# Kernel optimization log

Hardware: AMD Instinct MI355X
Metric: run time of the kernel (lower is better)

The kernel has to match this reference:

```python
import jax, jax.numpy as jnp
import numpy as np

B, S, D_EMBED, D_HIDDEN = 4, 256, 300, 300
C = 5.0  # frozen tanh-scaling constant


def setup_inputs() -> dict:
    key = jax.random.key(0)
    ks = jax.random.split(key, 8)
    w = 0.05  # ~xavier scale for 300x300
    return {
        "inputs": jax.random.normal(ks[0], (B, S, D_EMBED), jnp.float32),
        "rep_mask": jax.random.randint(ks[1], (B, S), 0, 2, jnp.int32),
        "W_fc": jax.random.normal(ks[2], (D_HIDDEN, D_EMBED), jnp.float32) * w,
        "b_fc": jnp.zeros((D_HIDDEN,), jnp.float32),
        "W1": jax.random.normal(ks[3], (D_HIDDEN, D_HIDDEN), jnp.float32) * w,
        "W2": jax.random.normal(ks[4], (D_HIDDEN, D_HIDDEN), jnp.float32) * w,
        "b1": jnp.zeros((D_HIDDEN,), jnp.float32),
        "W_f1": jax.random.normal(ks[5], (D_HIDDEN, D_HIDDEN), jnp.float32) * w,
        "W_f2": jax.random.normal(ks[6], (D_HIDDEN, D_HIDDEN), jnp.float32) * w,
        "b_f": jnp.zeros((D_HIDDEN,), jnp.float32),
    }


def _disa_fwd(inputs, rep_mask_f, W_fc, b_fc, W1, W2, b1, W_f1, W_f2, b_f):
    n_seq = inputs.shape[1]
    # forward direction mask: attend to strictly later positions (triu, diag=1)
    direct = jnp.triu(jnp.ones((n_seq, n_seq), inputs.dtype), k=1)
    # mask[b,i,j] = rep_mask[b,j] * direct[i,j], shape [B,S,S,1]
    mask = (rep_mask_f[:, None, :] * direct[None]) [..., None]

    rep_map = jax.nn.elu(jnp.einsum('bse,he->bsh', inputs, W_fc) + b_fc)  # [B,S,D]
    dep = jnp.einsum('bsh,gh->bsg', rep_map, W1)   # dependent (token j)
    head = jnp.einsum('bsh,gh->bsg', rep_map, W2)  # head (token i)

    # logits[b,i,j,d]
    logits = C * jnp.tanh((dep[:, None, :, :] + head[:, :, None, :] + b1) / C)

    # hand-rolled masked softmax over dim=2 (j), faithful to original
    masked = logits * mask
    mx = jnp.max(masked, axis=2, keepdims=True)
    exps = jnp.exp(masked - mx) * mask
    sums = jnp.sum(exps, axis=2, keepdims=True)
    sums = sums + (sums == 0).astype(logits.dtype)
    attn = (exps / (sums + 1e-20)) * mask

    attn_result = jnp.sum(attn * rep_map[:, None, :, :], axis=2)  # [B,S,D]

    gate = jax.nn.sigmoid(
        jnp.einsum('bsh,gh->bsg', rep_map, W_f1)
        + jnp.einsum('bsh,gh->bsg', attn_result, W_f2)
        + b_f
    )
    out = gate * rep_map + (1.0 - gate) * attn_result
    return out * rep_mask_f[..., None]


def reference(inputs, rep_mask, W_fc, b_fc, W1, W2, b1, W_f1, W_f2, b_f):
    rep_mask_f = rep_mask.astype(inputs.dtype)
    return _disa_fwd(inputs, rep_mask_f, W_fc, b_fc, W1, W2, b1, W_f1, W_f2, b_f)
```

## Files before the change

kernel.cpp:

```cpp
#include <hip/hip_runtime.h>
#include <hip/hip_bf16.h>

#define Dx 300

#define REPF   0
#define ED     307200
#define HEADF  921600
#define U_BASE 1228800
#define REPB   0
#define ATB    327680
#define WPACK  655360
#define WP1    655360
#define WP2    757760
#define WPF1   860160
#define WPF2   962560
#define ATTNF  1761280
#define SYNC_FOFF 2100000

typedef __attribute__((ext_vector_type(8))) short short8;
typedef __attribute__((ext_vector_type(4))) float f32x4;

union S8 { unsigned int u[4]; unsigned short s[8]; short8 v; };

__device__ __forceinline__ float bf2f(unsigned short u) {
    union { unsigned int i; float f; } v; v.i = ((unsigned int)u) << 16; return v.f;
}
__device__ __forceinline__ unsigned short f2bf(float x) {
    union { float f; unsigned int i; } u; u.f = x;
    return (unsigned short)((u.i + 0x8000u) >> 16);
}
__device__ __forceinline__ int detect_bf16(const void* w) {
    const unsigned short* u = (const unsigned short*)w;
    int ok = 1;
    #pragma unroll
    for (int t = 0; t < 64; ++t) { float v = bf2f(u[t]); ok &= (fabsf(v) < 1.0f) ? 1 : 0; }
    return ok;
}
__device__ __forceinline__ float ldf(const void* p, int idx, int isbf) {
    return isbf ? bf2f(((const unsigned short*)p)[idx]) : ((const float*)p)[idx];
}

__device__ __forceinline__ void st_wt_f32(float* p, float v) {
    asm volatile("global_store_dword %0, %1, off sc0 sc1"
                 :: "v"(p), "v"(v) : "memory");
}
__device__ __forceinline__ void st_wt_u16(unsigned short* p, unsigned short v) {
    unsigned int vv = v;
    asm volatile("global_store_short %0, %1, off sc0 sc1"
                 :: "v"(p), "v"(vv) : "memory");
}
__device__ __forceinline__ void st_wt_u32(void* p, unsigned int v) {
    asm volatile("global_store_dword %0, %1, off sc0 sc1"
                 :: "v"(p), "v"(v) : "memory");
}

__device__ __forceinline__ void load8f(const float* rowp, int kb, int kmax,
                                       int valid, float* x) {
    if (valid && kb + 8 <= kmax) {
        float4 a = *(const float4*)(rowp + kb);
        float4 b = *(const float4*)(rowp + kb + 4);
        x[0]=a.x; x[1]=a.y; x[2]=a.z; x[3]=a.w;
        x[4]=b.x; x[5]=b.y; x[6]=b.z; x[7]=b.w;
    } else {
        #pragma unroll
        for (int j = 0; j < 8; ++j) {
            int k = kb + j;
            x[j] = (valid && k < kmax) ? rowp[k] : 0.f;
        }
    }
}
__device__ __forceinline__ short8 pack8(const float* x) {
    S8 H;
    #pragma unroll
    for (int p = 0; p < 4; ++p) {
        union { float f; unsigned int i; } a, b;
        a.f = x[2*p]; b.f = x[2*p+1];
        H.u[p] = ((a.i + 0x8000u) >> 16) | ((b.i + 0x8000u) & 0xFFFF0000u);
    }
    return H.v;
}
__device__ __forceinline__ short8 load8bf(const unsigned short* rowp, int kb,
                                          int kmax, int valid) {
    S8 R;
    if (valid && kb + 8 <= kmax) {
        ushort4 a = *(const ushort4*)(rowp + kb);
        ushort4 b = *(const ushort4*)(rowp + kb + 4);
        R.s[0]=a.x; R.s[1]=a.y; R.s[2]=a.z; R.s[3]=a.w;
        R.s[4]=b.x; R.s[5]=b.y; R.s[6]=b.z; R.s[7]=b.w;
    } else {
        #pragma unroll
        for (int j = 0; j < 8; ++j) {
            int k = kb + j;
            R.s[j] = (valid && k < kmax) ? rowp[k] : (unsigned short)0;
        }
    }
    return R.v;
}
__device__ __forceinline__ short8 loadB(const void* W, int row, int kb, int isbf,
                                        int valid) {
    if (isbf) return load8bf((const unsigned short*)W + row * 300, kb, 300, valid);
    float t[8];
    load8f((const float*)W + row * 300, kb, 300, valid, t);
    return pack8(t);
}

#define AG __HIP_MEMORY_SCOPE_AGENT
__device__ __forceinline__ int xcd_id() {
    int x;
    asm volatile("s_getreg_b32 %0, hwreg(HW_REG_XCC_ID)" : "=s"(x));
    return x & 7;
}
__device__ __forceinline__ void gbar(float* ws, int idx, int nblk) {
    __syncthreads();
    if (threadIdx.x == 0) {
        int* base  = (int*)(ws + SYNC_FOFF) + idx * 2048;
        int* xcnt  = base;
        int* xflag = base + 8 * 64;
        const int xid = xcd_id();
        int t2 = __hip_atomic_fetch_add(xcnt + xid * 64, 1, __ATOMIC_RELAXED, AG);
        if (t2 == 0) {
            int t = 0;
            for (;;) {
                int s = 0;
                #pragma unroll
                for (int k = 0; k < 8; ++k)
                    s += __hip_atomic_load(xcnt + k * 64, __ATOMIC_RELAXED, AG);
                if (s >= nblk) break;
                __builtin_amdgcn_s_sleep(1);
                if (++t > 400000) break;
            }
            __hip_atomic_store(xflag + xid * 64, 1, __ATOMIC_RELAXED, AG);
        } else {
            int t = 0;
            while (__hip_atomic_load(xflag + xid * 64, __ATOMIC_RELAXED, AG) == 0) {
                __builtin_amdgcn_s_sleep(2);
                if (++t > 400000) break;
            }
        }
        asm volatile("" ::: "memory");
    }
    __syncthreads();
}

__global__ __launch_bounds__(320, 4) void k_a(
        const void* __restrict__ Xv, const void* __restrict__ Wfc,
        const void* __restrict__ bfc, const void* __restrict__ W1,
        const void* __restrict__ W2,  const void* __restrict__ b1v,
        const void* __restrict__ Wf1, const void* __restrict__ Wf2,
        float* __restrict__ ws) {
    __shared__ int s_isbf;
    const int tid = threadIdx.x;
    const int blk = blockIdx.x;
    if (tid == 0) s_isbf = detect_bf16(Wfc);
    __syncthreads();
    const int isbf = s_isbf;
    unsigned short* U = (unsigned short*)(ws + U_BASE);

    {
        const int g0 = blk * 640 + tid * 2;
        const int mi = g0 / 102400;
        const int rem = g0 - mi * 102400;
        const int row = rem / 320, k0 = rem - row * 320;
        const void* src = (mi == 0) ? W1 : (mi == 1) ? W2 : (mi == 2) ? Wf1 : Wf2;
        float v0 = (row < 300 && k0     < 300) ? ldf(src, row * 300 + k0,     isbf) : 0.f;
        float v1 = (row < 300 && k0 + 1 < 300) ? ldf(src, row * 300 + k0 + 1, isbf) : 0.f;
        unsigned int pk = (unsigned int)f2bf(v0) | ((unsigned int)f2bf(v1) << 16);
        st_wt_u32(U + WPACK + g0, pk);
    }
    if (blk < 320 && tid < 256) {
        const int w = tid >> 6, l = tid & 63;
        const int mt = blk / 5, nt = blk % 5;
        const int m0 = mt * 16, lm = l & 15, koff = (l >> 4) * 8;
        const int nrow = nt * 64 + w * 16 + lm;
        const int bval = nrow < 300;
        const int ncl = bval ? nrow : 0;
        f32x4 acc = {0.f, 0.f, 0.f, 0.f};
        if (isbf) {
            const unsigned short* Xp = (const unsigned short*)Xv + (m0 + lm) * 300;
            #pragma unroll
            for (int ks = 0; ks < 10; ++ks) {
                short8 a = load8bf(Xp, ks*32 + koff, 300, 1);
                short8 b = loadB(Wfc, ncl, ks*32 + koff, 1, bval);
                acc = __builtin_amdgcn_mfma_f32_16x16x32_bf16(a, b, acc, 0, 0, 0);
            }
        } else {
            const float* Xp = (const float*)Xv + (m0 + lm) * 300;
            #pragma unroll
            for (int ks = 0; ks < 10; ++ks) {
                float t[8]; load8f(Xp, ks*32 + koff, 300, 1, t);
                short8 a = pack8(t);
                short8 b = loadB(Wfc, ncl, ks*32 + koff, 0, bval);
                acc = __builtin_amdgcn_mfma_f32_16x16x32_bf16(a, b, acc, 0, 0, 0);
            }
        }
        if (bval) {
            float bb = ldf(bfc, nrow, isbf);
            #pragma unroll
            for (int r = 0; r < 4; ++r) {
                int mg = m0 + (l >> 4) * 4 + r;
                float v = acc[r] + bb;
                v = v > 0.f ? v : (__expf(v) - 1.f);
                ws[REPF + mg * 300 + nrow] = v;
                ws[ED + (mg * 300 + nrow) * 2 + 1] = v;
                st_wt_u16(U + REPB + mg * 320 + nrow, f2bf(v));
            }
        } else {
            #pragma unroll
            for (int r = 0; r < 4; ++r) {
                int mg = m0 + (l >> 4) * 4 + r;
                st_wt_u16(U + REPB + mg * 320 + nrow, 0);
            }
        }
    }
    gbar(ws, 0, 640);

    if (tid < 256) {
        const int w = tid >> 6, l = tid & 63;
        const int lm = l & 15, koff = (l >> 4) * 8;
        const int u = blk;
        const int mt = u / 10, nt = u % 10;
        const int m0 = mt * 16;
        const int ng = nt * 64 + w * 16 + lm;
        const int wsel = ng < 320;
        const int wrow = wsel ? ng : ng - 320;
        const unsigned short* ap = U + REPB + (m0 + lm) * 320 + koff;
        const unsigned short* bp = U + (wsel ? WP1 : WP2) + wrow * 320 + koff;
        f32x4 acc = {0.f, 0.f, 0.f, 0.f};
        #pragma unroll
        for (int ks = 0; ks < 10; ++ks) {
            short8 a = *(const short8*)(ap + ks * 32);
            short8 b = *(const short8*)(bp + ks * 32);
            acc = __builtin_amdgcn_mfma_f32_16x16x32_bf16(a, b, acc, 0, 0, 0);
        }
        if (ng < 300) {
            float bb = ldf(b1v, ng, isbf);
            #pragma unroll
            for (int r = 0; r < 4; ++r) {
                int mg = m0 + (l >> 4) * 4 + r;
                ws[ED + (mg * 300 + ng) * 2] = __expf(0.4f * (acc[r] + bb));
            }
        } else if (ng >= 320 && ng < 620) {
            #pragma unroll
            for (int r = 0; r < 4; ++r) {
                int mg = m0 + (l >> 4) * 4 + r;
                ws[HEADF + mg * 300 + (ng - 320)] = acc[r];
            }
        }
    }
}

__global__ __launch_bounds__(320, 4) void k_b(
        const int* __restrict__ mask, const void* __restrict__ Wfc,
        const void* __restrict__ bfv, float* __restrict__ ws,
        void* __restrict__ outv) {
    __shared__ int s_isbf;
    __shared__ unsigned short vlist[256];
    __shared__ int s_cnt, s_st0, s_st1;
    const int tid = threadIdx.x;
    const int blk = blockIdx.x;
    if (tid == 0) s_isbf = detect_bf16(Wfc);
    __syncthreads();
    const int isbf = s_isbf;
    unsigned short* U = (unsigned short*)(ws + U_BASE);

    {
        const int b = blk >> 7;
        const int tile = blk & 127;
        const int uu = tile >> 1;
        const int i0 = (tile & 1) ? (254 - 2 * uu) : (2 * uu);
        const int base = b * 256;
        const int mv0 = mask[base + i0] != 0;
        const int mv1 = mask[base + i0 + 1] != 0;
        if ((mv0 | mv1) && tid < 64) {
            int basec = 0, st0 = 0, st1 = 0;
            #pragma unroll
            for (int c = 0; c < 4; ++c) {
                const int j = c * 64 + tid;
                const int mv = mask[base + j] != 0;
                unsigned long long bal = __ballot(mv);
                int pos = basec + __popcll(bal & ((1ull << tid) - 1ull));
                if (mv) vlist[pos] = (unsigned short)j;
                if (tid == 0) {
                    int lim0 = i0 - c * 64;
                    if (lim0 >= 0)
                        st0 += __popcll(bal & (lim0 >= 63 ? ~0ull : ((2ull << lim0) - 1ull)));
                    int lim1 = i0 + 1 - c * 64;
                    if (lim1 >= 0)
                        st1 += __popcll(bal & (lim1 >= 63 ? ~0ull : ((2ull << lim1) - 1ull)));
                }
                basec += __popcll(bal);
            }
            if (tid == 0) { s_cnt = basec; s_st0 = st0; s_st1 = st1; }
        }
        __syncthreads();
        const int d = tid;
        if (d >= 300) {
            st_wt_u16(U + ATB + (base + i0) * 320 + d, 0);
            st_wt_u16(U + ATB + (base + i0 + 1) * 320 + d, 0);
        } else if (mv0 & mv1) {
            const int cnt = s_cnt, st0 = s_st0, st1 = s_st1;
            const float hv0 = ws[HEADF + (base + i0) * Dx + d];
            const float hv1 = ws[HEADF + (base + i0 + 1) * Dx + d];
            const float pw0 = __expf(0.4f * hv0);
            const float pw1 = __expf(0.4f * hv1);
            const float2* ep2 = ((const float2*)(ws + ED)) + base * Dx + d;
            float s0 = 0.f, r0 = 0.f, s1 = 0.f, r1 = 0.f;
            if (st1 > st0) {
                const int j = vlist[st0];
                float2 v = ep2[j * Dx];
                float u0 = fmaf(v.x, pw0, 1.0f);
                float e0 = __expf(-10.0f * __builtin_amdgcn_rcpf(u0));
                s0 += e0; r0 = fmaf(e0, v.y, r0);
            }
            #pragma unroll 8
            for (int t = st1; t < cnt; ++t) {
                const int j = vlist[t];
                float2 v = ep2[j * Dx];
                float u0 = fmaf(v.x, pw0, 1.0f);
                float u1 = fmaf(v.x, pw1, 1.0f);
                float e0 = __expf(-10.0f * __builtin_amdgcn_rcpf(u0));
                float e1 = __expf(-10.0f * __builtin_amdgcn_rcpf(u1));
                s0 += e0; r0 = fmaf(e0, v.y, r0);
                s1 += e1; r1 = fmaf(e1, v.y, r1);
            }
            const float den0 = s0 + (s0 == 0.f ? 1.f : 0.f) + 1e-20f;
            const float den1 = s1 + (s1 == 0.f ? 1.f : 0.f) + 1e-20f;
            const float a0 = r0 / den0, a1 = r1 / den1;
            st_wt_f32(ws + ATTNF + (base + i0) * Dx + d,     a0);
            st_wt_f32(ws + ATTNF + (base + i0 + 1) * Dx + d, a1);
            st_wt_u16(U + ATB + (base + i0) * 320 + d,     f2bf(a0));
            st_wt_u16(U + ATB + (base + i0 + 1) * 320 + d, f2bf(a1));
        } else if (mv0 | mv1) {
            const int cnt = s_cnt;
            const int ia  = mv0 ? i0 : (i0 + 1);
            const int sta = mv0 ? s_st0 : s_st1;
            const float hv = ws[HEADF + (base + ia) * Dx + d];
            const float pw = __expf(0.4f * hv);
            const float2* ep2 = ((const float2*)(ws + ED)) + base * Dx + d;
            float s = 0.f, r = 0.f;
            #pragma unroll 8
            for (int t = sta; t < cnt; ++t) {
                const int j = vlist[t];
                float2 v = ep2[j * Dx];
                float u0 = fmaf(v.x, pw, 1.0f);
                float e  = __expf(-10.0f * __builtin_amdgcn_rcpf(u0));
                s += e; r = fmaf(e, v.y, r);
            }
            const float den = s + (s == 0.f ? 1.f : 0.f) + 1e-20f;
            const float a = r / den;
            st_wt_f32(ws + ATTNF + (base + ia) * Dx + d, a);
            st_wt_u16(U + ATB + (base + ia) * 320 + d, f2bf(a));
        }
    }
    gbar(ws, 1, 512);

    if (blk < 320 && tid < 256) {
        const int w = tid >> 6, l = tid & 63;
        const int mt = blk / 5, nt = blk % 5;
        const int m0 = mt * 16, lm = l & 15, koff = (l >> 4) * 8;
        const int nrow = nt * 64 + w * 16 + lm;
        const unsigned short* a1p = U + REPB + (m0 + lm) * 320 + koff;
        const unsigned short* a2p = U + ATB  + (m0 + lm) * 320 + koff;
        const unsigned short* b1p = U + WPF1 + nrow * 320 + koff;
        const unsigned short* b2p = U + WPF2 + nrow * 320 + koff;
        f32x4 acc = {0.f, 0.f, 0.f, 0.f};
        #pragma unroll
        for (int ks = 0; ks < 10; ++ks) {
            short8 a = *(const short8*)(a1p + ks * 32);
            short8 b = *(const short8*)(b1p + ks * 32);
            acc = __builtin_amdgcn_mfma_f32_16x16x32_bf16(a, b, acc, 0, 0, 0);
        }
        #pragma unroll
        for (int ks = 0; ks < 10; ++ks) {
            short8 a = *(const short8*)(a2p + ks * 32);
            short8 b = *(const short8*)(b2p + ks * 32);
            acc = __builtin_amdgcn_mfma_f32_16x16x32_bf16(a, b, acc, 0, 0, 0);
        }
        if (nrow < 300) {
            float bb = ldf(bfv, nrow, isbf);
            #pragma unroll
            for (int r = 0; r < 4; ++r) {
                int mg = m0 + (l >> 4) * 4 + r;
                float res = 0.f;
                if (mask[mg]) {
                    float gp = acc[r] + bb;
                    float gate = 1.0f / (1.0f + __expf(-gp));
                    float rv = ws[REPF  + mg * 300 + nrow];
                    float av = ws[ATTNF + mg * 300 + nrow];
                    res = gate * rv + (1.0f - gate) * av;
                }
                if (isbf) ((__hip_bfloat16*)outv)[mg * 300 + nrow] = __float2bfloat16(res);
                else      ((float*)outv)[mg * 300 + nrow] = res;
            }
        }
    }
}

extern "C" void kernel_launch(void* const* d_in, const int* in_sizes, int n_in,
                              void* d_out, int out_size, void* d_ws, size_t ws_size,
                              hipStream_t stream) {
    const void* X   = d_in[0];
    const int*  msk = (const int*)d_in[1];
    const void* Wfc = d_in[2];
    const void* bfc = d_in[3];
    const void* W1  = d_in[4];
    const void* W2  = d_in[5];
    const void* b1  = d_in[6];
    const void* Wf1 = d_in[7];
    const void* Wf2 = d_in[8];
    const void* bfv = d_in[9];
    float* ws = (float*)d_ws;

    hipMemsetAsync((char*)d_ws + (size_t)SYNC_FOFF * sizeof(float), 0, 16384, stream);

    hipLaunchKernelGGL(k_a, dim3(640), dim3(320), 0, stream,
                       X, Wfc, bfc, W1, W2, b1, Wf1, Wf2, ws);
    hipLaunchKernelGGL(k_b, dim3(512), dim3(320), 0, stream,
                       msk, Wfc, bfv, ws, d_out);
}
```

Baseline: 127.2 us.

## Fuse two kernels into one with fine-grained dataflow counters instead of grid barriers

Merges the two launches into a single 512-block kernel and replaces the grid-wide barriers with per-row-tile and per-batch counters and flags. Blocks now start the next stage as soon as the tiles they depend on are ready. The weight pre-packing pass is dropped, and the W1/W2/Wf1/Wf2 GEMMs load and convert weights directly. The separate fp32 rep_map copy is also removed in favour of the interleaved buffer. This cuts launch overhead and barrier stalls, but adds extra on-the-fly weight conversion and relies on spin-waits, which assume co-resident blocks.

```diff
diff --git a/kernel.cpp b/kernel.cpp
--- a/kernel.cpp
+++ b/kernel.cpp
@@ -3,19 +3,15 @@
 
 #define Dx 300
 
-#define REPF   0
-#define ED     307200
-#define HEADF  921600
+#define ED     0
+#define HEADF  614400
+#define ATTNF  921600
 #define U_BASE 1228800
 #define REPB   0
 #define ATB    327680
-#define WPACK  655360
-#define WP1    655360
-#define WP2    757760
-#define WPF1   860160
-#define WPF2   962560
-#define ATTNF  1761280
-#define SYNC_FOFF 2100000
+#define SYNC_FOFF 2000000
+
+#define AG __HIP_MEMORY_SCOPE_AGENT
 
 typedef __attribute__((ext_vector_type(8))) short short8;
 typedef __attribute__((ext_vector_type(4))) float f32x4;
@@ -28,13 +24,6 @@
 __device__ __forceinline__ unsigned short f2bf(float x) {
     union { float f; unsigned int i; } u; u.f = x;
     return (unsigned short)((u.i + 0x8000u) >> 16);
-}
-__device__ __forceinline__ int detect_bf16(const void* w) {
-    const unsigned short* u = (const unsigned short*)w;
-    int ok = 1;
-    #pragma unroll
-    for (int t = 0; t < 64; ++t) { float v = bf2f(u[t]); ok &= (fabsf(v) < 1.0f) ? 1 : 0; }
-    return ok;
 }
 __device__ __forceinline__ float ldf(const void* p, int idx, int isbf) {
     return isbf ? bf2f(((const unsigned short*)p)[idx]) : ((const float*)p)[idx];
@@ -48,10 +37,6 @@
     unsigned int vv = v;
     asm volatile("global_store_short %0, %1, off sc0 sc1"
                  :: "v"(p), "v"(vv) : "memory");
-}
-__device__ __forceinline__ void st_wt_u32(void* p, unsigned int v) {
-    asm volatile("global_store_dword %0, %1, off sc0 sc1"
-                 :: "v"(p), "v"(v) : "memory");
 }
 
 __device__ __forceinline__ void load8f(const float* rowp, int kb, int kmax,
@@ -104,69 +89,46 @@
     return pack8(t);
 }
 
-#define AG __HIP_MEMORY_SCOPE_AGENT
 __device__ __forceinline__ int xcd_id() {
     int x;
     asm volatile("s_getreg_b32 %0, hwreg(HW_REG_XCC_ID)" : "=s"(x));
     return x & 7;
 }
-__device__ __forceinline__ void gbar(float* ws, int idx, int nblk) {
-    __syncthreads();
-    if (threadIdx.x == 0) {
-        int* base  = (int*)(ws + SYNC_FOFF) + idx * 2048;
-        int* xcnt  = base;
-        int* xflag = base + 8 * 64;
-        const int xid = xcd_id();
-        int t2 = __hip_atomic_fetch_add(xcnt + xid * 64, 1, __ATOMIC_RELAXED, AG);
-        if (t2 == 0) {
-            int t = 0;
-            for (;;) {
-                int s = 0;
-                #pragma unroll
-                for (int k = 0; k < 8; ++k)
-                    s += __hip_atomic_load(xcnt + k * 64, __ATOMIC_RELAXED, AG);
-                if (s >= nblk) break;
-                __builtin_amdgcn_s_sleep(1);
-                if (++t > 400000) break;
-            }
-            __hip_atomic_store(xflag + xid * 64, 1, __ATOMIC_RELAXED, AG);
-        } else {
-            int t = 0;
-            while (__hip_atomic_load(xflag + xid * 64, __ATOMIC_RELAXED, AG) == 0) {
-                __builtin_amdgcn_s_sleep(2);
-                if (++t > 400000) break;
-            }
-        }
-        asm volatile("" ::: "memory");
-    }
-    __syncthreads();
-}
-
-__global__ __launch_bounds__(320, 4) void k_a(
-        const void* __restrict__ Xv, const void* __restrict__ Wfc,
-        const void* __restrict__ bfc, const void* __restrict__ W1,
-        const void* __restrict__ W2,  const void* __restrict__ b1v,
-        const void* __restrict__ Wf1, const void* __restrict__ Wf2,
-        float* __restrict__ ws) {
+__device__ __forceinline__ void spin_ge(int* p, int target) {
+    int t = 0;
+    while (__hip_atomic_load(p, __ATOMIC_RELAXED, AG) < target) {
+        __builtin_amdgcn_s_sleep(2);
+        if (++t > 300000) break;
+    }
+    asm volatile("" ::: "memory");
+}
+
+
+__global__ __launch_bounds__(320, 4) void k_fused(
+        const void* __restrict__ Xv, const int* __restrict__ mask,
+        const void* __restrict__ Wfc, const void* __restrict__ bfc,
+        const void* __restrict__ W1,  const void* __restrict__ W2,
+        const void* __restrict__ b1v, const void* __restrict__ Wf1,
+        const void* __restrict__ Wf2, const void* __restrict__ bfv,
+        float* __restrict__ ws, void* __restrict__ outv) {
     __shared__ int s_isbf;
+    __shared__ unsigned short vlist[256];
+    __shared__ int s_cnt, s_st0, s_st1;
+
     const int tid = threadIdx.x;
     const int blk = blockIdx.x;
-    if (tid == 0) s_isbf = detect_bf16(Wfc);
+    if (tid < 64) {
+        float v = bf2f(((const unsigned short*)Wfc)[tid]);
+        int ok = fabsf(v) < 1.0f;
+        unsigned long long bal = __ballot(ok);
+        if (tid == 0) s_isbf = (bal == ~0ull) ? 1 : 0;
+    }
     __syncthreads();
     const int isbf = s_isbf;
     unsigned short* U = (unsigned short*)(ws + U_BASE);
-
-    {
-        const int g0 = blk * 640 + tid * 2;
-        const int mi = g0 / 102400;
-        const int rem = g0 - mi * 102400;
-        const int row = rem / 320, k0 = rem - row * 320;
-        const void* src = (mi == 0) ? W1 : (mi == 1) ? W2 : (mi == 2) ? Wf1 : Wf2;
-        float v0 = (row < 300 && k0     < 300) ? ldf(src, row * 300 + k0,     isbf) : 0.f;
-        float v1 = (row < 300 && k0 + 1 < 300) ? ldf(src, row * 300 + k0 + 1, isbf) : 0.f;
-        unsigned int pk = (unsigned int)f2bf(v0) | ((unsigned int)f2bf(v1) << 16);
-        st_wt_u32(U + WPACK + g0, pk);
-    }
+    int* S = (int*)(ws + SYNC_FOFF);
+    const int xid = xcd_id();
+
     if (blk < 320 && tid < 256) {
         const int w = tid >> 6, l = tid & 63;
         const int mt = blk / 5, nt = blk % 5;
@@ -200,8 +162,7 @@
                 int mg = m0 + (l >> 4) * 4 + r;
                 float v = acc[r] + bb;
                 v = v > 0.f ? v : (__expf(v) - 1.f);
-                ws[REPF + mg * 300 + nrow] = v;
-                ws[ED + (mg * 300 + nrow) * 2 + 1] = v;
+                st_wt_f32(ws + ED + (mg * 300 + nrow) * 2 + 1, v);
                 st_wt_u16(U + REPB + mg * 320 + nrow, f2bf(v));
             }
         } else {
@@ -212,63 +173,75 @@
             }
         }
     }
-    gbar(ws, 0, 640);
-
-    if (tid < 256) {
-        const int w = tid >> 6, l = tid & 63;
-        const int lm = l & 15, koff = (l >> 4) * 8;
-        const int u = blk;
-        const int mt = u / 10, nt = u % 10;
-        const int m0 = mt * 16;
-        const int ng = nt * 64 + w * 16 + lm;
-        const int wsel = ng < 320;
-        const int wrow = wsel ? ng : ng - 320;
-        const unsigned short* ap = U + REPB + (m0 + lm) * 320 + koff;
-        const unsigned short* bp = U + (wsel ? WP1 : WP2) + wrow * 320 + koff;
-        f32x4 acc = {0.f, 0.f, 0.f, 0.f};
-        #pragma unroll
-        for (int ks = 0; ks < 10; ++ks) {
-            short8 a = *(const short8*)(ap + ks * 32);
-            short8 b = *(const short8*)(bp + ks * 32);
-            acc = __builtin_amdgcn_mfma_f32_16x16x32_bf16(a, b, acc, 0, 0, 0);
-        }
-        if (ng < 300) {
-            float bb = ldf(b1v, ng, isbf);
-            #pragma unroll
-            for (int r = 0; r < 4; ++r) {
-                int mg = m0 + (l >> 4) * 4 + r;
-                ws[ED + (mg * 300 + ng) * 2] = __expf(0.4f * (acc[r] + bb));
-            }
-        } else if (ng >= 320 && ng < 620) {
-            #pragma unroll
-            for (int r = 0; r < 4; ++r) {
-                int mg = m0 + (l >> 4) * 4 + r;
-                ws[HEADF + mg * 300 + (ng - 320)] = acc[r];
-            }
-        }
-    }
-}
-
-__global__ __launch_bounds__(320, 4) void k_b(
-        const int* __restrict__ mask, const void* __restrict__ Wfc,
-        const void* __restrict__ bfv, float* __restrict__ ws,
-        void* __restrict__ outv) {
-    __shared__ int s_isbf;
-    __shared__ unsigned short vlist[256];
-    __shared__ int s_cnt, s_st0, s_st1;
-    const int tid = threadIdx.x;
-    const int blk = blockIdx.x;
-    if (tid == 0) s_isbf = detect_bf16(Wfc);
     __syncthreads();
-    const int isbf = s_isbf;
-    unsigned short* U = (unsigned short*)(ws + U_BASE);
+    if (blk < 320 && tid == 0)
+        __hip_atomic_fetch_add(S + (blk / 5) * 64, 1, __ATOMIC_RELAXED, AG);
 
     {
-        const int b = blk >> 7;
-        const int tile = blk & 127;
-        const int uu = tile >> 1;
-        const int i0 = (tile & 1) ? (254 - 2 * uu) : (2 * uu);
-        const int base = b * 256;
+        int u0 = blk;
+        int u1 = (blk >= 320 && blk < 448) ? 512 + (blk - 320) : -1;
+        for (int q = 0; q < 2; ++q) {
+            const int u = (q == 0) ? u0 : u1;
+            if (u < 0) break;
+            const int mt = u / 10, nt = u % 10;
+            if (tid == 0) spin_ge(S + mt * 64, 5);
+            __syncthreads();
+            if (tid < 256) {
+                const int w = tid >> 6, l = tid & 63;
+                const int m0 = mt * 16, lm = l & 15, koff = (l >> 4) * 8;
+                const int ng = nt * 64 + w * 16 + lm;
+                const int wsel = ng < 320;
+                const int wrow = wsel ? ng : ng - 320;
+                const int bval = wrow < 300;
+                const int ncl = bval ? wrow : 0;
+                const void* Wsel = wsel ? W1 : W2;
+                const unsigned short* ap = U + REPB + (m0 + lm) * 320 + koff;
+                f32x4 acc = {0.f, 0.f, 0.f, 0.f};
+                #pragma unroll
+                for (int ks = 0; ks < 10; ++ks) {
+                    short8 a = *(const short8*)(ap + ks * 32);
+                    short8 b = loadB(Wsel, ncl, ks*32 + koff, isbf, bval);
+                    acc = __builtin_amdgcn_mfma_f32_16x16x32_bf16(a, b, acc, 0, 0, 0);
+                }
+                if (ng < 300) {
+                    float bb = ldf(b1v, ng, isbf);
+                    #pragma unroll
+                    for (int r = 0; r < 4; ++r) {
+                        int mg = m0 + (l >> 4) * 4 + r;
+                        st_wt_f32(ws + ED + (mg * 300 + ng) * 2,
+                                  __expf(0.4f * (acc[r] + bb)));
+                    }
+                } else if (ng >= 320 && ng < 620) {
+                    #pragma unroll
+                    for (int r = 0; r < 4; ++r) {
+                        int mg = m0 + (l >> 4) * 4 + r;
+                        st_wt_f32(ws + HEADF + mg * 300 + (ng - 320), acc[r]);
+                    }
+                }
+            }
+            __syncthreads();
+            if (tid == 0) {
+                const int bb = mt >> 4;
+                int old = __hip_atomic_fetch_add(S + (64 + bb) * 64, 1,
+                                                 __ATOMIC_RELAXED, AG);
+                if (old == 159) {
+                    #pragma unroll
+                    for (int x = 0; x < 8; ++x)
+                        __hip_atomic_store(S + (68 + bb * 8 + x) * 64, 1,
+                                           __ATOMIC_RELAXED, AG);
+                }
+            }
+        }
+    }
+
+    const int b = blk >> 7;
+    const int tile = blk & 127;
+    const int uu = tile >> 1;
+    const int i0 = (tile & 1) ? (254 - 2 * uu) : (2 * uu);
+    const int base = b * 256;
+    if (tid == 0) spin_ge(S + (68 + b * 8 + xid) * 64, 1);
+    __syncthreads();
+    {
         const int mv0 = mask[base + i0] != 0;
         const int mv1 = mask[base + i0 + 1] != 0;
         if ((mv0 | mv1) && tid < 64) {
@@ -352,45 +325,53 @@
             st_wt_u16(U + ATB + (base + ia) * 320 + d, f2bf(a));
         }
     }
-    gbar(ws, 1, 512);
-
-    if (blk < 320 && tid < 256) {
-        const int w = tid >> 6, l = tid & 63;
-        const int mt = blk / 5, nt = blk % 5;
-        const int m0 = mt * 16, lm = l & 15, koff = (l >> 4) * 8;
-        const int nrow = nt * 64 + w * 16 + lm;
-        const unsigned short* a1p = U + REPB + (m0 + lm) * 320 + koff;
-        const unsigned short* a2p = U + ATB  + (m0 + lm) * 320 + koff;
-        const unsigned short* b1p = U + WPF1 + nrow * 320 + koff;
-        const unsigned short* b2p = U + WPF2 + nrow * 320 + koff;
-        f32x4 acc = {0.f, 0.f, 0.f, 0.f};
-        #pragma unroll
-        for (int ks = 0; ks < 10; ++ks) {
-            short8 a = *(const short8*)(a1p + ks * 32);
-            short8 b = *(const short8*)(b1p + ks * 32);
-            acc = __builtin_amdgcn_mfma_f32_16x16x32_bf16(a, b, acc, 0, 0, 0);
-        }
-        #pragma unroll
-        for (int ks = 0; ks < 10; ++ks) {
-            short8 a = *(const short8*)(a2p + ks * 32);
-            short8 b = *(const short8*)(b2p + ks * 32);
-            acc = __builtin_amdgcn_mfma_f32_16x16x32_bf16(a, b, acc, 0, 0, 0);
-        }
-        if (nrow < 300) {
-            float bb = ldf(bfv, nrow, isbf);
-            #pragma unroll
-            for (int r = 0; r < 4; ++r) {
-                int mg = m0 + (l >> 4) * 4 + r;
-                float res = 0.f;
-                if (mask[mg]) {
-                    float gp = acc[r] + bb;
-                    float gate = 1.0f / (1.0f + __expf(-gp));
-                    float rv = ws[REPF  + mg * 300 + nrow];
-                    float av = ws[ATTNF + mg * 300 + nrow];
-                    res = gate * rv + (1.0f - gate) * av;
-                }
-                if (isbf) ((__hip_bfloat16*)outv)[mg * 300 + nrow] = __float2bfloat16(res);
-                else      ((float*)outv)[mg * 300 + nrow] = res;
+    __syncthreads();
+    if (tid == 0)
+        __hip_atomic_fetch_add(S + (100 + ((base + i0) >> 4)) * 64, 1,
+                               __ATOMIC_RELAXED, AG);
+
+    if (blk >= 192) {
+        const int u = blk - 192;
+        const int mt3 = u / 5, nt3 = u % 5;
+        if (tid == 0) spin_ge(S + (100 + mt3) * 64, 8);
+        __syncthreads();
+        if (tid < 256) {
+            const int w = tid >> 6, l = tid & 63;
+            const int m0 = mt3 * 16, lm = l & 15, koff = (l >> 4) * 8;
+            const int nrow = nt3 * 64 + w * 16 + lm;
+            const int bval = nrow < 300;
+            const int ncl = bval ? nrow : 0;
+            const unsigned short* a1p = U + REPB + (m0 + lm) * 320 + koff;
+            const unsigned short* a2p = U + ATB  + (m0 + lm) * 320 + koff;
+            f32x4 acc = {0.f, 0.f, 0.f, 0.f};
+            #pragma unroll
+            for (int ks = 0; ks < 10; ++ks) {
+                short8 a = *(const short8*)(a1p + ks * 32);
+                short8 bB = loadB(Wf1, ncl, ks*32 + koff, isbf, bval);
+                acc = __builtin_amdgcn_mfma_f32_16x16x32_bf16(a, bB, acc, 0, 0, 0);
+            }
+            #pragma unroll
+            for (int ks = 0; ks < 10; ++ks) {
+                short8 a = *(const short8*)(a2p + ks * 32);
+                short8 bB = loadB(Wf2, ncl, ks*32 + koff, isbf, bval);
+                acc = __builtin_amdgcn_mfma_f32_16x16x32_bf16(a, bB, acc, 0, 0, 0);
+            }
+            if (bval) {
+                float bb = ldf(bfv, nrow, isbf);
+                #pragma unroll
+                for (int r = 0; r < 4; ++r) {
+                    int mg = m0 + (l >> 4) * 4 + r;
+                    float res = 0.f;
+                    if (mask[mg]) {
+                        float gp = acc[r] + bb;
+                        float gate = 1.0f / (1.0f + __expf(-gp));
+                        float rv = ws[ED + (mg * 300 + nrow) * 2 + 1];
+                        float av = ws[ATTNF + mg * 300 + nrow];
+                        res = gate * rv + (1.0f - gate) * av;
+                    }
+                    if (isbf) ((__hip_bfloat16*)outv)[mg * 300 + nrow] = __float2bfloat16(res);
+                    else      ((float*)outv)[mg * 300 + nrow] = res;
+                }
             }
         }
     }
@@ -411,10 +392,8 @@
     const void* bfv = d_in[9];
     float* ws = (float*)d_ws;
 
-    hipMemsetAsync((char*)d_ws + (size_t)SYNC_FOFF * sizeof(float), 0, 16384, stream);
-
-    hipLaunchKernelGGL(k_a, dim3(640), dim3(320), 0, stream,
-                       X, Wfc, bfc, W1, W2, b1, Wf1, Wf2, ws);
-    hipLaunchKernelGGL(k_b, dim3(512), dim3(320), 0, stream,
-                       msk, Wfc, bfv, ws, d_out);
-}
+    hipMemsetAsync((char*)d_ws + (size_t)SYNC_FOFF * sizeof(float), 0, 49152, stream);
+
+    hipLaunchKernelGGL(k_fused, dim3(512), dim3(320), 0, stream,
+                       X, msk, Wfc, bfc, W1, W2, b1, Wf1, Wf2, bfv, ws, d_out);
+}
```

New measurement: 119.5 us. -6.0%, faster.
